# Performance work log

Hardware: AMD Instinct MI355X
Metric: run time of the kernel (lower is better)

Reference implementation:

```python
import jax, jax.numpy as jnp
import numpy as np

HIDDEN = 2560
HEADS = 32
HEAD_DIM = HIDDEN // HEADS  # 80
ROT = HEAD_DIM // 2         # partial_rotary_factor=0.5 -> 40
B = 2
S = 2048
T = B * S
THETA = 10000.0


def setup_inputs() -> dict:
    key = jax.random.key(0)
    k0, k1, k2, k3, k4 = jax.random.split(key, 5)
    hidden_states = jax.random.normal(k0, (T, HIDDEN), jnp.float32)
    w_qkv = jax.random.normal(k1, (3 * HIDDEN, HIDDEN), jnp.float32) * 0.02
    b_qkv = jax.random.normal(k2, (3 * HIDDEN,), jnp.float32) * 0.02
    w_o = jax.random.normal(k3, (HIDDEN, HIDDEN), jnp.float32) * 0.02
    b_o = jax.random.normal(k4, (HIDDEN,), jnp.float32) * 0.02
    # rotary tables for positions 0..S-1 per sequence, rotary_dim=ROT
    pos = jnp.tile(jnp.arange(S, dtype=jnp.float32), B)  # [T]
    inv_freq = 1.0 / (THETA ** (jnp.arange(0, ROT, 2, dtype=jnp.float32) / ROT))  # [ROT//2]
    freqs = pos[:, None] * inv_freq[None, :]  # [T, ROT//2]
    return {
        "hidden_states": hidden_states,
        "w_qkv": w_qkv,
        "b_qkv": b_qkv,
        "w_o": w_o,
        "b_o": b_o,
        "cos": jnp.cos(freqs),
        "sin": jnp.sin(freqs),
        "batch": B,
    }


def _apply_rope(x, cos, sin):
    # x: [T, H, D]; rotate first ROT dims NeoX-style (rotate_half)
    half = ROT // 2
    x1 = x[..., :half]
    x2 = x[..., half:ROT]
    c = cos[:, None, :]
    s = sin[:, None, :]
    return jnp.concatenate([x1 * c - x2 * s, x1 * s + x2 * c, x[..., ROT:]], axis=-1)


def reference(hidden_states, w_qkv, b_qkv, w_o, b_o, cos, sin, batch):
    t, hdim = hidden_states.shape
    seq = t // batch
    # fused QKV projection (with bias)
    qkv = hidden_states @ w_qkv.T + b_qkv  # [T, 3*HIDDEN]
    q, k, v = jnp.split(qkv, 3, axis=1)
    q = _apply_rope(q.reshape(t, HEADS, HEAD_DIM), cos, sin)
    k = _apply_rope(k.reshape(t, HEADS, HEAD_DIM), cos, sin)
    v = v.reshape(t, HEADS, HEAD_DIM)
    # prefill causal attention per sequence
    qb = q.reshape(batch, seq, HEADS, HEAD_DIM)
    kb = k.reshape(batch, seq, HEADS, HEAD_DIM)
    vb = v.reshape(batch, seq, HEADS, HEAD_DIM)
    scale = 1.0 / jnp.sqrt(jnp.float32(HEAD_DIM))
    scores = jnp.einsum("bqhd,bkhd->bhqk", qb, kb) * scale  # [B,H,S,S]
    causal = jnp.tril(jnp.ones((seq, seq), dtype=bool))
    scores = jnp.where(causal[None, None], scores, jnp.finfo(scores.dtype).min)
    attn = jax.nn.softmax(scores, axis=-1)
    out = jnp.einsum("bhqk,bkhd->bqhd", attn, vb).reshape(t, HIDDEN)
    return out @ w_o.T + b_o
```

## Files before the change

### kernel.cpp

```cpp
#include <hip/hip_runtime.h>
#include <hip/hip_bf16.h>

#define HID   2560
#define NH    32
#define HD    80
#define SEQ   2048
#define TTOT  4096
#define QKVN  7680

typedef float  f32x4  __attribute__((ext_vector_type(4)));
typedef short  short8 __attribute__((ext_vector_type(8)));
typedef __bf16 bf16x8 __attribute__((ext_vector_type(8)));
typedef __hip_bfloat16 bf16;

__device__ __forceinline__ float bf2f(bf16 h) { return __bfloat162float(h); }
__device__ __forceinline__ bf16  f2bf(float f) { return __float2bfloat16(f); }

__device__ __forceinline__ f32x4 mfma16(short8 a, short8 b, f32x4 c) {
  return __builtin_amdgcn_mfma_f32_16x16x32_bf16(
      __builtin_bit_cast(bf16x8, a), __builtin_bit_cast(bf16x8, b), c, 0, 0, 0);
}

typedef __attribute__((address_space(1))) const unsigned int as1_uint;
typedef __attribute__((address_space(3))) unsigned int       as3_uint;
__device__ __forceinline__ void gld16(const void* g, void* l) {
  __builtin_amdgcn_global_load_lds((as1_uint*)g, (as3_uint*)l, 16, 0, 0);
}

__global__ void detect_kernel(const unsigned short* __restrict__ hid, int* flag) {
  const int tid = threadIdx.x;
  const unsigned short u = hid[2 * (tid * 997)];
  const int e = (u >> 7) & 0xFF;
  const int sane = (u == 0 || (e >= 0x60 && e <= 0x8A)) ? 1 : 0;
  __shared__ int cnt;
  if (tid == 0) cnt = 0;
  __syncthreads();
  atomicAdd(&cnt, sane);
  __syncthreads();
  if (tid == 0) *flag = (cnt < 160) ? 1 : 0;
}

__global__ void convert_kernel(const void* __restrict__ src, bf16* __restrict__ dst,
                               int n8, const int* __restrict__ flag) {
  const bool isf32 = (*flag != 0);
  for (int i = blockIdx.x * 256 + threadIdx.x; i < n8; i += gridDim.x * 256) {
    if (isf32) {
      const float4* s = (const float4*)src;
      float4 a = s[2 * i], b = s[2 * i + 1];
      __align__(16) bf16 o8[8] = {f2bf(a.x), f2bf(a.y), f2bf(a.z), f2bf(a.w),
                                  f2bf(b.x), f2bf(b.y), f2bf(b.z), f2bf(b.w)};
      *(uint4*)(dst + 8 * i) = *(const uint4*)o8;
    } else {
      *(uint4*)(dst + 8 * i) = ((const uint4*)src)[i];
    }
  }
}

__global__ void emit_kernel(const bf16* __restrict__ src, void* __restrict__ dst,
                            int n8, const int* __restrict__ flag) {
  const bool isf32 = (*flag != 0);
  for (int i = blockIdx.x * 256 + threadIdx.x; i < n8; i += gridDim.x * 256) {
    uint4 v = *(const uint4*)(src + 8 * i);
    if (isf32) {
      const bf16* b = (const bf16*)&v;
      float4* d = (float4*)dst;
      d[2 * i]     = make_float4(bf2f(b[0]), bf2f(b[1]), bf2f(b[2]), bf2f(b[3]));
      d[2 * i + 1] = make_float4(bf2f(b[4]), bf2f(b[5]), bf2f(b[6]), bf2f(b[7]));
    } else {
      ((uint4*)dst)[i] = v;
    }
  }
}

__global__ __launch_bounds__(512, 2) void gemm256_bias(
    const bf16* __restrict__ A, const bf16* __restrict__ B,
    const bf16* __restrict__ bias, bf16* __restrict__ C,
    int M, int N, int K)
{
  __shared__ __align__(16) bf16 lA[3][16384];
  __shared__ __align__(16) bf16 lB[2][16384];

  const int tid  = threadIdx.x;
  const int wid  = tid >> 6;
  const int lane = tid & 63;
  const int quad = lane >> 4;
  const int l15  = lane & 15;
  const int wr   = wid >> 2;
  const int wc   = wid & 3;

  int wgid;
  {
    const int nwg = gridDim.x;
    const int q = nwg >> 3, r = nwg & 7;
    const int xcd = blockIdx.x & 7, lin = blockIdx.x >> 3;
    wgid = (xcd < r ? xcd * (q + 1) : r * (q + 1) + (xcd - r) * q) + lin;
  }
  const int gx = M >> 8;
  const int m0 = (wgid % gx) << 8;
  const int n0 = (wgid / gx) << 8;

  const int NT = K >> 6;

  const int rr   = tid >> 3;
  const int cbyt = ((tid & 7) << 4) ^ ((rr & 7) << 4);
  const size_t o1 = (size_t)rr * K + (cbyt >> 1);
  const size_t o2 = o1 + (size_t)64 * K;

  const bf16* Ab = A + (size_t)m0 * K;
  const bf16* Bb = B + (size_t)n0 * K;

#define STAGEA(bufsel, half, tt)                                               \
  {                                                                            \
    const bf16* _s = Ab + (size_t)(half) * 128 * K + (tt) * 64;                \
    bf16* _d = &lA[bufsel][(half) * 8192 + wid * 512];                         \
    gld16(_s + o1, _d);                                                        \
    gld16(_s + o2, _d + 4096);                                                 \
  }
#define STAGEB(bufsel, half, tt)                                               \
  {                                                                            \
    const bf16* _s = Bb + (size_t)(half) * 128 * K + (tt) * 64;                \
    bf16* _d = &lB[bufsel][(half) * 8192 + wid * 512];                         \
    gld16(_s + o1, _d);                                                        \
    gld16(_s + o2, _d + 4096);                                                 \
  }

  const int csw0 = ((quad ^ (l15 & 7)) << 4);
  const int csw1 = (((4 | quad) ^ (l15 & 7)) << 4);

  f32x4 acc[8][4];
#pragma unroll
  for (int i = 0; i < 8; ++i)
#pragma unroll
    for (int j = 0; j < 4; ++j) acc[i][j] = (f32x4)0.f;

  short8 a[4][2], b[4][2];

  STAGEA(0, 0, 0); STAGEA(0, 1, 0);
  STAGEB(0, 0, 0); STAGEB(0, 1, 0);
  STAGEA(1, 0, 1); STAGEA(1, 1, 1);
  STAGEB(1, 0, 1); STAGEB(1, 1, 1);
  asm volatile("s_waitcnt vmcnt(8)" ::: "memory");
  __builtin_amdgcn_s_barrier();

  for (int t = 0; t < NT; ++t) {
    const int ac  = t % 3;
    const int an2 = (t + 2) % 3;
    const int bc  = t & 1;
    const bf16* Al = lA[ac];
    const bf16* Bl = lB[bc];
    const bool pf = (t + 2 < NT);

#pragma unroll
    for (int mi = 0; mi < 4; ++mi) {
      const char* p = (const char*)Al + (size_t)(wr * 128 + mi * 16 + l15) * 128;
      a[mi][0] = *(const short8*)(p + csw0);
      a[mi][1] = *(const short8*)(p + csw1);
    }
#pragma unroll
    for (int n = 0; n < 2; ++n) {
      const char* p = (const char*)Bl + (size_t)(wc * 64 + n * 16 + l15) * 128;
      b[n][0] = *(const short8*)(p + csw0);
      b[n][1] = *(const short8*)(p + csw1);
    }
    if (pf) STAGEA(an2, 0, t + 2);
    __builtin_amdgcn_s_barrier();
    asm volatile("s_waitcnt lgkmcnt(0)" ::: "memory");
    __builtin_amdgcn_sched_barrier(0);
    __builtin_amdgcn_s_setprio(1);
#pragma unroll
    for (int mi = 0; mi < 4; ++mi)
#pragma unroll
      for (int n = 0; n < 2; ++n) {
        acc[mi][n] = mfma16(a[mi][0], b[n][0], acc[mi][n]);
        acc[mi][n] = mfma16(a[mi][1], b[n][1], acc[mi][n]);
      }
    __builtin_amdgcn_s_setprio(0);
    __builtin_amdgcn_s_barrier();

#pragma unroll
    for (int n = 2; n < 4; ++n) {
      const char* p = (const char*)Bl + (size_t)(wc * 64 + n * 16 + l15) * 128;
      b[n][0] = *(const short8*)(p + csw0);
      b[n][1] = *(const short8*)(p + csw1);
    }
    if (pf) STAGEA(an2, 1, t + 2);
    __builtin_amdgcn_s_barrier();
    asm volatile("s_waitcnt lgkmcnt(0)" ::: "memory");
    __builtin_amdgcn_sched_barrier(0);
    __builtin_amdgcn_s_setprio(1);
#pragma unroll
    for (int mi = 0; mi < 4; ++mi)
#pragma unroll
      for (int n = 2; n < 4; ++n) {
        acc[mi][n] = mfma16(a[mi][0], b[n][0], acc[mi][n]);
        acc[mi][n] = mfma16(a[mi][1], b[n][1], acc[mi][n]);
      }
    __builtin_amdgcn_s_setprio(0);
    __builtin_amdgcn_s_barrier();

#pragma unroll
    for (int mi = 0; mi < 4; ++mi) {
      const char* p = (const char*)Al + (size_t)(wr * 128 + 64 + mi * 16 + l15) * 128;
      a[mi][0] = *(const short8*)(p + csw0);
      a[mi][1] = *(const short8*)(p + csw1);
    }
    if (pf) STAGEB(bc, 0, t + 2);
    __builtin_amdgcn_s_barrier();
    asm volatile("s_waitcnt lgkmcnt(0)" ::: "memory");
    __builtin_amdgcn_sched_barrier(0);
    __builtin_amdgcn_s_setprio(1);
#pragma unroll
    for (int mi = 0; mi < 4; ++mi)
#pragma unroll
      for (int n = 2; n < 4; ++n) {
        acc[4 + mi][n] = mfma16(a[mi][0], b[n][0], acc[4 + mi][n]);
        acc[4 + mi][n] = mfma16(a[mi][1], b[n][1], acc[4 + mi][n]);
      }
    __builtin_amdgcn_s_setprio(0);
    __builtin_amdgcn_s_barrier();

    if (pf) STAGEB(bc, 1, t + 2);
    __builtin_amdgcn_s_barrier();
    __builtin_amdgcn_s_setprio(1);
#pragma unroll
    for (int mi = 0; mi < 4; ++mi)
#pragma unroll
      for (int n = 0; n < 2; ++n) {
        acc[4 + mi][n] = mfma16(a[mi][0], b[n][0], acc[4 + mi][n]);
        acc[4 + mi][n] = mfma16(a[mi][1], b[n][1], acc[4 + mi][n]);
      }
    __builtin_amdgcn_s_setprio(0);
    if (pf) {
      asm volatile("s_waitcnt vmcnt(8)" ::: "memory");
    } else if (t + 1 < NT) {
      asm volatile("s_waitcnt vmcnt(0)" ::: "memory");
    }
    __builtin_amdgcn_s_barrier();
  }
#undef STAGEA
#undef STAGEB

  const int crow = m0 + wr * 128 + quad * 4;
  const int ccol = n0 + wc * 64 + l15;
#pragma unroll
  for (int n = 0; n < 4; ++n) {
    const float bv = bf2f(bias[ccol + n * 16]);
#pragma unroll
    for (int mi = 0; mi < 8; ++mi) {
      const int rb = crow + mi * 16;
#pragma unroll
      for (int r = 0; r < 4; ++r)
        C[(size_t)(rb + r) * N + ccol + n * 16] = f2bf(acc[mi][n][r] + bv);
    }
  }
}

__global__ __launch_bounds__(256) void rope_kernel(
    const bf16* __restrict__ qkv, const bf16* __restrict__ cosb,
    const bf16* __restrict__ sinb, bf16* __restrict__ Qr, bf16* __restrict__ Kr)
{
  const int t = blockIdx.x;
  const int b = t >> 11;
  const int s = t & 2047;
  const float qscale = 0.11180339887498949f;

  __shared__ float cs[20], sn[20];
  if (threadIdx.x < 20) cs[threadIdx.x] = bf2f(cosb[t * 20 + threadIdx.x]);
  if (threadIdx.x >= 32 && threadIdx.x < 52)
    sn[threadIdx.x - 32] = bf2f(sinb[t * 20 + (threadIdx.x - 32)]);
  __syncthreads();

  const bf16* qrow = qkv + (size_t)t * QKVN;
  const bf16* krow = qrow + HID;

  for (int idx = threadIdx.x; idx < HID; idx += 256) {
    const int h = idx / HD, d = idx % HD;
    const size_t off = ((size_t)(b * NH + h) * SEQ + s) * HD + d;
    float q, k;
    if (d < 20) {
      q = bf2f(qrow[h * HD + d]) * cs[d] - bf2f(qrow[h * HD + d + 20]) * sn[d];
      k = bf2f(krow[h * HD + d]) * cs[d] - bf2f(krow[h * HD + d + 20]) * sn[d];
    } else if (d < 40) {
      q = bf2f(qrow[h * HD + d - 20]) * sn[d - 20] + bf2f(qrow[h * HD + d]) * cs[d - 20];
      k = bf2f(krow[h * HD + d - 20]) * sn[d - 20] + bf2f(krow[h * HD + d]) * cs[d - 20];
    } else {
      q = bf2f(qrow[h * HD + d]);
      k = bf2f(krow[h * HD + d]);
    }
    Qr[off] = f2bf(q * qscale);
    Kr[off] = f2bf(k);
  }
}

__global__ __launch_bounds__(256) void vtrans_kernel(
    const bf16* __restrict__ qkv, bf16* __restrict__ Vt)
{
  const int bh = blockIdx.x;
  const int s0 = blockIdx.y * 64;
  const int b = bh >> 5, h = bh & 31;
  __shared__ bf16 tile[64][81];

  for (int e = threadIdx.x; e < 64 * HD; e += 256) {
    const int r = e / HD, d = e % HD;
    tile[r][d] = qkv[(size_t)(b * SEQ + s0 + r) * QKVN + 2 * HID + h * HD + d];
  }
  __syncthreads();
  for (int e = threadIdx.x; e < 64 * HD; e += 256) {
    const int d = e >> 6, r = e & 63;
    Vt[((size_t)bh * HD + d) * SEQ + s0 + r] = tile[r][d];
  }
}

__global__ __launch_bounds__(256, 3) void attn_kernel(
    const bf16* __restrict__ Qr, const bf16* __restrict__ Kr,
    const bf16* __restrict__ Vt, bf16* __restrict__ O)
{
  const int raw  = blockIdx.x;
  const int slot = raw >> 3;
  const int qblk = 15 - (slot & 15);
  const int bh   = ((slot >> 4) << 3) + (raw & 7);

  const int tid  = threadIdx.x;
  const int wave = tid >> 6;
  const int lane = tid & 63;
  const int quad = lane >> 4;
  const int l15  = lane & 15;
  const int qbase = qblk * 128;

  __shared__ __align__(16) bf16 stage[12544];
  __shared__ __align__(16) bf16 pt[4 * 2 * 1152];

  bf16* kt = stage;
  bf16* vt = stage + 5632;

  if (tid < 144) {
    const unsigned one2 = 0x3F803F80u;
    *(uint4*)&vt[5760 + tid * 8] = (uint4){one2, one2, one2, one2};
  }

  int goff[6];
#pragma unroll
  for (int it = 0; it < 6; it++) {
    const int j = tid + it * 256;
    if (j < 704) {
      const int r = j / 11; int c = j - 11 * r; if (c > 9) c = 0;
      goff[it] = r * 160 + c * 16;
    } else {
      const int j2 = j - 704;
      const int r = j2 / 9; int c = j2 - 9 * r; if (c > 7) c = 0;
      goff[it] = r * 4096 + c * 16;
    }
  }

  short8 aq[2][3];
#pragma unroll
  for (int f = 0; f < 2; f++) {
    const bf16* Qb = Qr + ((size_t)bh * SEQ + qbase + f * 64 + wave * 16 + l15) * HD + quad * 8;
    aq[f][0] = *(const short8*)(Qb);
    aq[f][1] = *(const short8*)(Qb + 32);
    aq[f][2] = *(const short8*)(Qb + 64);
    if (quad >= 2) aq[f][2] = (short8)0;
  }

  f32x4 o[2][6];
#pragma unroll
  for (int f = 0; f < 2; f++)
    for (int nt = 0; nt < 6; nt++) o[f][nt] = (f32x4)0.f;
  float m_i[2] = {-3e38f, -3e38f};

  const char* Kb8 = (const char*)(Kr + (size_t)bh * SEQ * HD);
  const char* Vb8 = (const char*)(Vt + (size_t)bh * HD * SEQ);
  const int nsteps = 2 * qblk + 2;
  const int rmax0 = qbase + wave * 16 + 15;

  for (int step = 0; step < nsteps; step++) {
    const int kvo = step * 64;
    const bool act0 = (kvo <= rmax0);

    __syncthreads();
    {
      const char* kb = Kb8 + kvo * 160;
      const char* vb = Vb8 + kvo * 2;
#pragma unroll
      for (int it = 0; it < 6; it++) {
        const int j = tid + it * 256;
        if (j < 1424) {
          bf16* ldsb = stage + (it * 256 + wave * 64) * 8;
          gld16((j < 704) ? (kb + goff[it]) : (vb + goff[it]), ldsb);
        }
      }
    }
    __syncthreads();

    f32x4 sv[2][4];
#pragma unroll
    for (int nt = 0; nt < 4; nt++) {
      const bf16* kr = &kt[(nt * 16 + l15) * 88 + quad * 8];
      short8 b0 = *(const short8*)(kr);
      short8 b1 = *(const short8*)(kr + 32);
      short8 b2 = *(const short8*)(kr + 64);
      if (act0) {
        f32x4 s = mfma16(b0, aq[0][0], (f32x4)0.f);
        s = mfma16(b1, aq[0][1], s);
        sv[0][nt] = mfma16(b2, aq[0][2], s);
      }
      f32x4 s1 = mfma16(b0, aq[1][0], (f32x4)0.f);
      s1 = mfma16(b1, aq[1][1], s1);
      sv[1][nt] = mfma16(b2, aq[1][2], s1);
    }

#pragma unroll
    for (int f = 0; f < 2; f++) {
      if (f == 0 && !act0) continue;
      const int mrel = qbase + f * 64 + wave * 16 - kvo;
      if (mrel < 63) {
        const int qrel = mrel + l15;
#pragma unroll
        for (int nt = 0; nt < 4; nt++) {
          f32x4 t = sv[f][nt];
#pragma unroll
          for (int r = 0; r < 4; r++)
            t[r] = (nt * 16 + quad * 4 + r <= qrel) ? t[r] : -3e38f;
          sv[f][nt] = t;
        }
      }
      float mx = fmaxf(fmaxf(sv[f][0][0], sv[f][0][1]), fmaxf(sv[f][0][2], sv[f][0][3]));
#pragma unroll
      for (int nt = 1; nt < 4; nt++)
        mx = fmaxf(mx, fmaxf(fmaxf(sv[f][nt][0], sv[f][nt][1]),
                             fmaxf(sv[f][nt][2], sv[f][nt][3])));
      mx = fmaxf(mx, __shfl_xor(mx, 16, 64));
      mx = fmaxf(mx, __shfl_xor(mx, 32, 64));
      const float mnew = fmaxf(m_i[f], mx);
      const float alpha = __expf(m_i[f] - mnew);
      m_i[f] = mnew;

      bf16* ptw = pt + (wave * 2 + f) * 1152;
#pragma unroll
      for (int nt = 0; nt < 4; nt++) {
        __align__(8) bf16 p4[4];
#pragma unroll
        for (int r = 0; r < 4; r++) p4[r] = f2bf(__expf(sv[f][nt][r] - mnew));
        *(unsigned long long*)&ptw[l15 * 72 + nt * 16 + quad * 4] =
            *(const unsigned long long*)p4;
      }
      float av[4];
#pragma unroll
      for (int r = 0; r < 4; r++) av[r] = __shfl(alpha, quad * 4 + r, 64);
#pragma unroll
      for (int nt = 0; nt < 6; nt++) {
        f32x4 t = o[f][nt];
        t[0] *= av[0]; t[1] *= av[1]; t[2] *= av[2]; t[3] *= av[3];
        o[f][nt] = t;
      }
    }

    asm volatile("s_waitcnt lgkmcnt(0)" ::: "memory");
    short8 pa00 = (short8)0, pa01 = (short8)0, pa10, pa11;
    {
      const bf16* p0 = pt + (wave * 2 + 0) * 1152 + l15 * 72 + quad * 8;
      const bf16* p1 = pt + (wave * 2 + 1) * 1152 + l15 * 72 + quad * 8;
      if (act0) { pa00 = *(const short8*)p0; pa01 = *(const short8*)(p0 + 32); }
      pa10 = *(const short8*)p1; pa11 = *(const short8*)(p1 + 32);
    }
#pragma unroll
    for (int nt = 0; nt < 6; nt++) {
      const bf16* vr = &vt[(nt * 16 + l15) * 72 + quad * 8];
      short8 v0 = *(const short8*)(vr);
      short8 v1 = *(const short8*)(vr + 32);
      if (act0) {
        o[0][nt] = mfma16(pa00, v0, o[0][nt]);
        o[0][nt] = mfma16(pa01, v1, o[0][nt]);
      }
      o[1][nt] = mfma16(pa10, v0, o[1][nt]);
      o[1][nt] = mfma16(pa11, v1, o[1][nt]);
    }
  }

  const int b = bh >> 5, h = bh & 31;
#pragma unroll
  for (int f = 0; f < 2; f++)
#pragma unroll
    for (int r = 0; r < 4; r++) {
      const float inv = 1.0f / o[f][5][r];
      const int trow = b * SEQ + qbase + f * 64 + wave * 16 + quad * 4 + r;
#pragma unroll
      for (int nt = 0; nt < 5; nt++)
        O[(size_t)trow * HID + h * HD + nt * 16 + l15] = f2bf(o[f][nt][r] * inv);
    }
}

extern "C" void kernel_launch(void* const* d_in, const int* in_sizes, int n_in,
                              void* d_out, int out_size, void* d_ws, size_t ws_size,
                              hipStream_t stream) {
  (void)in_sizes; (void)n_in; (void)ws_size;
  char* wsb = (char*)d_ws;

  int*  flag   = (int*) (wsb + 0);
  bf16* cos_c  = (bf16*)(wsb + 1024);
  bf16* sin_c  = (bf16*)(wsb + 165888);
  bf16* bqkv_c = (bf16*)(wsb + 329728);
  bf16* bo_c   = (bf16*)(wsb + 345088);
  bf16* wo_c   = (bf16*)(wsb + 1048576);
  bf16* qkv    = (bf16*)(wsb + 14155776);
  bf16* hid_c  = (bf16*)(wsb + 77070336);
  bf16* wqkv_c = (bf16*)(wsb + 98041856);
  bf16* Qr     = (bf16*)(wsb + 77070336);
  bf16* Kr     = (bf16*)(wsb + 98041856);
  bf16* Vt     = (bf16*)(wsb + 119013376);
  bf16* attn   = (bf16*)(wsb + 14155776);
  bf16* obuf   = (bf16*)(wsb + 35127296);

  detect_kernel<<<1, 256, 0, stream>>>((const unsigned short*)d_in[0], flag);
  convert_kernel<<<1024, 256, 0, stream>>>(d_in[0], hid_c,  TTOT * HID / 8, flag);
  convert_kernel<<<1024, 256, 0, stream>>>(d_in[1], wqkv_c, QKVN * HID / 8, flag);
  convert_kernel<<<4,    256, 0, stream>>>(d_in[2], bqkv_c, QKVN / 8,       flag);
  convert_kernel<<<1024, 256, 0, stream>>>(d_in[3], wo_c,   HID * HID / 8,  flag);
  convert_kernel<<<2,    256, 0, stream>>>(d_in[4], bo_c,   HID / 8,        flag);
  convert_kernel<<<40,   256, 0, stream>>>(d_in[5], cos_c,  TTOT * 20 / 8,  flag);
  convert_kernel<<<40,   256, 0, stream>>>(d_in[6], sin_c,  TTOT * 20 / 8,  flag);

  gemm256_bias<<<dim3((TTOT / 256) * (QKVN / 256)), 512, 0, stream>>>(
      hid_c, wqkv_c, bqkv_c, qkv, TTOT, QKVN, HID);
  rope_kernel<<<dim3(TTOT), 256, 0, stream>>>(qkv, cos_c, sin_c, Qr, Kr);
  vtrans_kernel<<<dim3(64, SEQ / 64), 256, 0, stream>>>(qkv, Vt);
  attn_kernel<<<dim3(1024), 256, 0, stream>>>(Qr, Kr, Vt, attn);
  gemm256_bias<<<dim3((TTOT / 256) * (HID / 256)), 512, 0, stream>>>(
      attn, wo_c, bo_c, obuf, TTOT, HID, HID);
  emit_kernel<<<1024, 256, 0, stream>>>(obuf, d_out, out_size / 8, flag);
}
```

Measured before the change: 605.9 us.

## Software-pipeline LDS fragment loads across k-tiles in GEMM with partial lgkm waits

Restructures the bf16 MFMA GEMM main loop so that LDS fragment reads for the next k-tile (A rows 0-63 and B cols 0-31) are issued before the last MFMA phases of the current tile. Double-buffered B01 registers let the loop unroll by two, and partial lgkmcnt waits replace full drains. The number of workgroup barriers per k-tile drops from eight to two. The goal is to hide LDS latency behind MFMA work and cut synchronisation stalls, at the cost of more VGPR pressure and more delicate buffer-reuse ordering.

```diff
diff --git a/kernel.cpp b/kernel.cpp
--- a/kernel.cpp
+++ b/kernel.cpp
@@ -111,19 +111,26 @@
 
 #define STAGEA(bufsel, half, tt)                                               \
   {                                                                            \
-    const bf16* _s = Ab + (size_t)(half) * 128 * K + (tt) * 64;                \
+    const bf16* _s = Ab + (size_t)(half) * 128 * K + (size_t)(tt) * 64;        \
     bf16* _d = &lA[bufsel][(half) * 8192 + wid * 512];                         \
     gld16(_s + o1, _d);                                                        \
     gld16(_s + o2, _d + 4096);                                                 \
   }
 #define STAGEB(bufsel, half, tt)                                               \
   {                                                                            \
-    const bf16* _s = Bb + (size_t)(half) * 128 * K + (tt) * 64;                \
+    const bf16* _s = Bb + (size_t)(half) * 128 * K + (size_t)(tt) * 64;        \
     bf16* _d = &lB[bufsel][(half) * 8192 + wid * 512];                         \
     gld16(_s + o1, _d);                                                        \
     gld16(_s + o2, _d + 4096);                                                 \
   }
 
+#define WAIT_LGKM(n)                                                           \
+  do {                                                                         \
+    asm volatile("s_waitcnt lgkmcnt(" #n ")" ::: "memory");                    \
+    __builtin_amdgcn_sched_barrier(0);                                         \
+  } while (0)
+#define WAIT_VM(n) asm volatile("s_waitcnt vmcnt(" #n ")" ::: "memory")
+
   const int csw0 = ((quad ^ (l15 & 7)) << 4);
   const int csw1 = (((4 | quad) ^ (l15 & 7)) << 4);
 
@@ -133,112 +140,117 @@
 #pragma unroll
     for (int j = 0; j < 4; ++j) acc[i][j] = (f32x4)0.f;
 
-  short8 a[4][2], b[4][2];
+  short8 a03[4][2], a47[4][2], b23[2][2], b01A[2][2], b01B[2][2];
 
   STAGEA(0, 0, 0); STAGEA(0, 1, 0);
   STAGEB(0, 0, 0); STAGEB(0, 1, 0);
-  STAGEA(1, 0, 1); STAGEA(1, 1, 1);
-  STAGEB(1, 0, 1); STAGEB(1, 1, 1);
-  asm volatile("s_waitcnt vmcnt(8)" ::: "memory");
+  if (NT > 1) {
+    STAGEA(1, 0, 1); STAGEA(1, 1, 1);
+    STAGEB(1, 0, 1); STAGEB(1, 1, 1);
+    WAIT_VM(8);
+  } else {
+    WAIT_VM(0);
+  }
   __builtin_amdgcn_s_barrier();
-
-  for (int t = 0; t < NT; ++t) {
-    const int ac  = t % 3;
-    const int an2 = (t + 2) % 3;
-    const int bc  = t & 1;
-    const bf16* Al = lA[ac];
-    const bf16* Bl = lB[bc];
-    const bool pf = (t + 2 < NT);
-
-#pragma unroll
-    for (int mi = 0; mi < 4; ++mi) {
-      const char* p = (const char*)Al + (size_t)(wr * 128 + mi * 16 + l15) * 128;
-      a[mi][0] = *(const short8*)(p + csw0);
-      a[mi][1] = *(const short8*)(p + csw1);
-    }
-#pragma unroll
-    for (int n = 0; n < 2; ++n) {
-      const char* p = (const char*)Bl + (size_t)(wc * 64 + n * 16 + l15) * 128;
-      b[n][0] = *(const short8*)(p + csw0);
-      b[n][1] = *(const short8*)(p + csw1);
-    }
-    if (pf) STAGEA(an2, 0, t + 2);
-    __builtin_amdgcn_s_barrier();
-    asm volatile("s_waitcnt lgkmcnt(0)" ::: "memory");
-    __builtin_amdgcn_sched_barrier(0);
-    __builtin_amdgcn_s_setprio(1);
-#pragma unroll
-    for (int mi = 0; mi < 4; ++mi)
-#pragma unroll
-      for (int n = 0; n < 2; ++n) {
-        acc[mi][n] = mfma16(a[mi][0], b[n][0], acc[mi][n]);
-        acc[mi][n] = mfma16(a[mi][1], b[n][1], acc[mi][n]);
-      }
-    __builtin_amdgcn_s_setprio(0);
-    __builtin_amdgcn_s_barrier();
-
-#pragma unroll
-    for (int n = 2; n < 4; ++n) {
-      const char* p = (const char*)Bl + (size_t)(wc * 64 + n * 16 + l15) * 128;
-      b[n][0] = *(const short8*)(p + csw0);
-      b[n][1] = *(const short8*)(p + csw1);
-    }
-    if (pf) STAGEA(an2, 1, t + 2);
-    __builtin_amdgcn_s_barrier();
-    asm volatile("s_waitcnt lgkmcnt(0)" ::: "memory");
-    __builtin_amdgcn_sched_barrier(0);
-    __builtin_amdgcn_s_setprio(1);
-#pragma unroll
-    for (int mi = 0; mi < 4; ++mi)
-#pragma unroll
-      for (int n = 2; n < 4; ++n) {
-        acc[mi][n] = mfma16(a[mi][0], b[n][0], acc[mi][n]);
-        acc[mi][n] = mfma16(a[mi][1], b[n][1], acc[mi][n]);
-      }
-    __builtin_amdgcn_s_setprio(0);
-    __builtin_amdgcn_s_barrier();
-
-#pragma unroll
-    for (int mi = 0; mi < 4; ++mi) {
-      const char* p = (const char*)Al + (size_t)(wr * 128 + 64 + mi * 16 + l15) * 128;
-      a[mi][0] = *(const short8*)(p + csw0);
-      a[mi][1] = *(const short8*)(p + csw1);
-    }
-    if (pf) STAGEB(bc, 0, t + 2);
-    __builtin_amdgcn_s_barrier();
-    asm volatile("s_waitcnt lgkmcnt(0)" ::: "memory");
-    __builtin_amdgcn_sched_barrier(0);
-    __builtin_amdgcn_s_setprio(1);
-#pragma unroll
-    for (int mi = 0; mi < 4; ++mi)
-#pragma unroll
-      for (int n = 2; n < 4; ++n) {
-        acc[4 + mi][n] = mfma16(a[mi][0], b[n][0], acc[4 + mi][n]);
-        acc[4 + mi][n] = mfma16(a[mi][1], b[n][1], acc[4 + mi][n]);
-      }
-    __builtin_amdgcn_s_setprio(0);
-    __builtin_amdgcn_s_barrier();
-
-    if (pf) STAGEB(bc, 1, t + 2);
-    __builtin_amdgcn_s_barrier();
-    __builtin_amdgcn_s_setprio(1);
-#pragma unroll
-    for (int mi = 0; mi < 4; ++mi)
-#pragma unroll
-      for (int n = 0; n < 2; ++n) {
-        acc[4 + mi][n] = mfma16(a[mi][0], b[n][0], acc[4 + mi][n]);
-        acc[4 + mi][n] = mfma16(a[mi][1], b[n][1], acc[4 + mi][n]);
-      }
-    __builtin_amdgcn_s_setprio(0);
-    if (pf) {
-      asm volatile("s_waitcnt vmcnt(8)" ::: "memory");
-    } else if (t + 1 < NT) {
-      asm volatile("s_waitcnt vmcnt(0)" ::: "memory");
-    }
-    __builtin_amdgcn_s_barrier();
-  }
+#pragma unroll
+  for (int mi = 0; mi < 4; ++mi) {
+    const char* p = (const char*)lA[0] + (size_t)(wr * 128 + mi * 16 + l15) * 128;
+    a03[mi][0] = *(const short8*)(p + csw0);
+    a03[mi][1] = *(const short8*)(p + csw1);
+  }
+#pragma unroll
+  for (int n = 0; n < 2; ++n) {
+    const char* p = (const char*)lB[0] + (size_t)(wc * 64 + n * 16 + l15) * 128;
+    b01A[n][0] = *(const short8*)(p + csw0);
+    b01A[n][1] = *(const short8*)(p + csw1);
+  }
+
+#define KTILE(T, B01U, B01L)                                                   \
+  do {                                                                         \
+    const int _t = (T);                                                        \
+    const bf16* Al = lA[_t % 3];                                               \
+    const bf16* Bl = lB[_t & 1];                                               \
+    const bool stg = (_t + 2 < NT);                                            \
+    const bool nxt = (_t + 1 < NT);                                            \
+     \
+    if (stg) STAGEA((_t + 2) % 3, 0, _t + 2);                                  \
+    _Pragma("unroll") for (int n = 0; n < 2; ++n) {                            \
+      const char* p = (const char*)Bl + (size_t)(wc * 64 + (2 + n) * 16 + l15) * 128; \
+      b23[n][0] = *(const short8*)(p + csw0);                                  \
+      b23[n][1] = *(const short8*)(p + csw1);                                  \
+    }                                                                          \
+    WAIT_LGKM(4);                                                              \
+    __builtin_amdgcn_s_setprio(1);                                             \
+    _Pragma("unroll") for (int mi = 0; mi < 4; ++mi)                           \
+      _Pragma("unroll") for (int n = 0; n < 2; ++n) {                          \
+        acc[mi][n] = mfma16(a03[mi][0], B01U[n][0], acc[mi][n]);               \
+        acc[mi][n] = mfma16(a03[mi][1], B01U[n][1], acc[mi][n]);               \
+      }                                                                        \
+    __builtin_amdgcn_s_setprio(0);                                             \
+             \
+    if (stg) STAGEA((_t + 2) % 3, 1, _t + 2);                                  \
+    _Pragma("unroll") for (int mi = 0; mi < 4; ++mi) {                         \
+      const char* p = (const char*)Al + (size_t)(wr * 128 + 64 + mi * 16 + l15) * 128; \
+      a47[mi][0] = *(const short8*)(p + csw0);                                 \
+      a47[mi][1] = *(const short8*)(p + csw1);                                 \
+    }                                                                          \
+    WAIT_LGKM(8);                                                              \
+    __builtin_amdgcn_s_setprio(1);                                             \
+    _Pragma("unroll") for (int mi = 0; mi < 4; ++mi)                           \
+      _Pragma("unroll") for (int n = 0; n < 2; ++n) {                          \
+        acc[mi][2 + n] = mfma16(a03[mi][0], b23[n][0], acc[mi][2 + n]);        \
+        acc[mi][2 + n] = mfma16(a03[mi][1], b23[n][1], acc[mi][2 + n]);        \
+      }                                                                        \
+    __builtin_amdgcn_s_setprio(0);                                             \
+                                             \
+    if (stg) { WAIT_VM(4); } else { WAIT_VM(0); }                              \
+    __builtin_amdgcn_s_barrier();                                              \
+    if (stg) STAGEB(_t & 1, 0, _t + 2);                                        \
+    if (nxt) {                                                                 \
+      const bf16* Aln = lA[(_t + 1) % 3];                                      \
+      const bf16* Bln = lB[(_t + 1) & 1];                                      \
+      _Pragma("unroll") for (int mi = 0; mi < 4; ++mi) {                       \
+        const char* p = (const char*)Aln + (size_t)(wr * 128 + mi * 16 + l15) * 128; \
+        a03[mi][0] = *(const short8*)(p + csw0);                               \
+        a03[mi][1] = *(const short8*)(p + csw1);                               \
+      }                                                                        \
+      _Pragma("unroll") for (int n = 0; n < 2; ++n) {                          \
+        const char* p = (const char*)Bln + (size_t)(wc * 64 + n * 16 + l15) * 128; \
+        B01L[n][0] = *(const short8*)(p + csw0);                               \
+        B01L[n][1] = *(const short8*)(p + csw1);                               \
+      }                                                                        \
+      WAIT_LGKM(12);                                                           \
+    } else {                                                                   \
+      WAIT_LGKM(0);                                                            \
+    }                                                                          \
+    __builtin_amdgcn_s_setprio(1);                                             \
+    _Pragma("unroll") for (int mi = 0; mi < 4; ++mi)                           \
+      _Pragma("unroll") for (int n = 0; n < 2; ++n) {                          \
+        acc[4 + mi][2 + n] = mfma16(a47[mi][0], b23[n][0], acc[4 + mi][2 + n]); \
+        acc[4 + mi][2 + n] = mfma16(a47[mi][1], b23[n][1], acc[4 + mi][2 + n]); \
+      }                                                                        \
+    __builtin_amdgcn_s_setprio(0);                                             \
+      \
+    __builtin_amdgcn_s_barrier();                                              \
+    if (stg) STAGEB(_t & 1, 1, _t + 2);                                        \
+    __builtin_amdgcn_s_setprio(1);                                             \
+    _Pragma("unroll") for (int mi = 0; mi < 4; ++mi)                           \
+      _Pragma("unroll") for (int n = 0; n < 2; ++n) {                          \
+        acc[4 + mi][n] = mfma16(a47[mi][0], B01U[n][0], acc[4 + mi][n]);       \
+        acc[4 + mi][n] = mfma16(a47[mi][1], B01U[n][1], acc[4 + mi][n]);       \
+      }                                                                        \
+    __builtin_amdgcn_s_setprio(0);                                             \
+  } while (0)
+
+  for (int t = 0; t < NT; t += 2) {
+    KTILE(t, b01A, b01B);
+    if (t + 1 < NT) KTILE(t + 1, b01B, b01A);
+  }
+#undef KTILE
 #undef STAGEA
 #undef STAGEB
+#undef WAIT_LGKM
+#undef WAIT_VM
 
   const int crow = m0 + wr * 128 + quad * 4;
   const int ccol = n0 + wc * 64 + l15;
```

After: 805.7 us. +33.0%, slower.
